# Performance work log

Measured on AMD Instinct MI355X. Metric: run time of the kernel, lower is better.

The kernel has to match this reference:

```python
import jax, jax.numpy as jnp
import numpy as np

MEM_DIM = 128  # GRU hidden / memory dim
EMB_DIM = 512  # encoder embedding dim (jk_out_channels)
N_ACTIVE = 200000
MAX_NODES = 250000
OUT_CH = 2


def setup_inputs() -> dict:
    key = jax.random.key(0)
    ks = jax.random.split(key, 8)
    s_ih = 1.0 / np.sqrt(MEM_DIM)
    return {
        "embeddings": jax.random.normal(ks[0], (N_ACTIVE, EMB_DIM), jnp.float32),
        "node_ids": jnp.arange(N_ACTIVE, dtype=jnp.int64 if jax.config.jax_enable_x64 else jnp.int32),
        "memory_bank": jax.random.normal(ks[1], (MAX_NODES, MEM_DIM), jnp.float32),
        "W_ih": jax.random.uniform(ks[2], (3 * MEM_DIM, EMB_DIM), jnp.float32, -s_ih, s_ih),
        "W_hh": jax.random.uniform(ks[3], (3 * MEM_DIM, MEM_DIM), jnp.float32, -s_ih, s_ih),
        "b_ih": jax.random.uniform(ks[4], (3 * MEM_DIM,), jnp.float32, -s_ih, s_ih),
        "b_hh": jax.random.uniform(ks[5], (3 * MEM_DIM,), jnp.float32, -s_ih, s_ih),
        "W_cls": jax.random.uniform(ks[6], (OUT_CH, EMB_DIM + MEM_DIM), jnp.float32, -1.0 / np.sqrt(EMB_DIM + MEM_DIM), 1.0 / np.sqrt(EMB_DIM + MEM_DIM)),
        "b_cls": jax.random.uniform(ks[7], (OUT_CH,), jnp.float32, -1.0 / np.sqrt(EMB_DIM + MEM_DIM), 1.0 / np.sqrt(EMB_DIM + MEM_DIM)),
    }


def gru_cell(x, h, W_ih, W_hh, b_ih, b_hh):
    # torch.nn.GRUCell math. x: [N, E], h: [N, M]
    gi = x @ W_ih.T + b_ih                 # [N, 3M]
    gh = h @ W_hh.T + b_hh                 # [N, 3M]
    i_r, i_z, i_n = jnp.split(gi, 3, axis=1)
    h_r, h_z, h_n = jnp.split(gh, 3, axis=1)
    r = jax.nn.sigmoid(i_r + h_r)
    z = jax.nn.sigmoid(i_z + h_z)
    n = jnp.tanh(i_n + r * h_n)
    return (1.0 - z) * n + z * h


def reference(embeddings, node_ids, memory_bank, W_ih, W_hh, b_ih, b_hh, W_cls, b_cls):
    # gather per-node memory
    prev_mem = memory_bank[node_ids]                       # [N, M]
    # GRUCell update
    new_mem = gru_cell(embeddings, prev_mem, W_ih, W_hh, b_ih, b_hh)
    # scatter back (detached in the original)
    updated_bank = memory_bank.at[node_ids].set(jax.lax.stop_gradient(new_mem))
    # concat + linear classify (dropout is identity at eval)
    combined = jnp.concatenate([embeddings, new_mem], axis=1)  # [N, E+M]
    logits = combined @ W_cls.T + b_cls                        # [N, out]
    return logits, updated_bank
```

## Files before the change

kernel.cpp:

```cpp
#include <hip/hip_runtime.h>
#include <hip/hip_bf16.h>

typedef short short8 __attribute__((ext_vector_type(8)));
typedef float f32x4  __attribute__((ext_vector_type(4)));

#define EMB   512
#define MEM   128
#define G3    384
#define CLS_K 640
#define KJ    640
#define BK    32
#define NKS   20
#define ROWS  64
#define NTHR  512
#define WB_CLS (G3 * KJ)

__device__ __forceinline__ short f2b(float f) {
  __hip_bfloat16 h = __float2bfloat16(f);
  return __builtin_bit_cast(short, h);
}
__device__ __forceinline__ short8 cvt8(f32x4 a, f32x4 b) {
  short8 v;
  v[0] = f2b(a[0]); v[1] = f2b(a[1]); v[2] = f2b(a[2]); v[3] = f2b(a[3]);
  v[4] = f2b(b[0]); v[5] = f2b(b[1]); v[6] = f2b(b[2]); v[7] = f2b(b[3]);
  return v;
}
__device__ __forceinline__ float sigm(float x)     { return 1.f / (1.f + __expf(-x)); }
__device__ __forceinline__ float tanhfast(float x) { return 2.f / (1.f + __expf(-2.f * x)) - 1.f; }

__device__ __forceinline__ void gll16(const void* gsrc, void* ldst) {
  __builtin_amdgcn_global_load_lds(
      (const __attribute__((address_space(1))) unsigned int*)gsrc,
      (__attribute__((address_space(3))) unsigned int*)ldst, 16, 0, 0);
}

__global__ void prep_w_kernel(const float* __restrict__ wih, const float* __restrict__ whh,
                              const float* __restrict__ wcls, short* __restrict__ outw) {
  int i = blockIdx.x * blockDim.x + threadIdx.x;
  const int nJ = G3 * KJ;
  const int nTot = nJ + 2 * EMB;
  if (i < nJ) {
    const int col = i / KJ, k = i - col * KJ;
    const float v = (k < EMB) ? wih[(size_t)col * EMB + k] : whh[(size_t)col * MEM + (k - EMB)];
    outw[i] = f2b(v);
  } else if (i < nTot) {
    const int j = i - nJ;
    const int r = j >> 9, k = j & 511;
    outw[i] = f2b(wcls[(size_t)r * CLS_K + k]);
  }
}

__global__ void bitmap_set_kernel(const int* __restrict__ ids, unsigned char* __restrict__ bm, int n) {
  int i = blockIdx.x * blockDim.x + threadIdx.x;
  if (i < n) bm[ids[i]] = 1;
}

__global__ void copy_bank_kernel(const f32x4* __restrict__ src, f32x4* __restrict__ dst,
                                 const unsigned char* __restrict__ bm, int n4) {
  int i = blockIdx.x * blockDim.x + threadIdx.x;
  int stride = gridDim.x * blockDim.x;
  for (; i < n4; i += stride) {
    if (bm && bm[i >> 5]) continue;
    dst[i] = src[i];
  }
}

template <bool BF16W>
__global__ __launch_bounds__(NTHR, 4)
void fused_gru_kernel(const float* __restrict__ emb, const int* __restrict__ ids,
                      const float* __restrict__ bank,
                      const float* __restrict__ Wihf, const float* __restrict__ Whhf,
                      const float* __restrict__ bih,  const float* __restrict__ bhh,
                      const float* __restrict__ Wcls, const float* __restrict__ bcls,
                      const short* __restrict__ Wb,
                      float* __restrict__ out_logits, float* __restrict__ out_bank, int N) {
  __shared__ __align__(16) float sA[2][ROWS * BK];
  __shared__ __align__(16) short sB[2][G3 * BK];
  __shared__ __align__(16) short sCls[2 * EMB];

  const int t    = threadIdx.x;
  const int lane = t & 63;
  const int w    = t >> 6;
  const int wr   = w & 3;
  const int wc   = w >> 2;
  const int lr   = lane & 15;
  const int lk   = lane >> 4;
  const int r0   = blockIdx.x * ROWS;

  const int rowS = w * 8 + (lane >> 3);
  const int schS = (lane & 7) ^ (rowS & 7);
  int growS = r0 + rowS; if (growS > N - 1) growS = N - 1;
  const int gidS = ids[growS];
  const char* pEmbS  = (const char*)(emb  + (size_t)growS * EMB) + schS * 16;
  const char* pBankS = (const char*)(bank + (size_t)gidS  * MEM) + schS * 16;

  int bOff[3];
#pragma unroll
  for (int s = 0; s < 3; ++s) {
    const int cB = s * 512 + w * 64 + lane;
    const int cp = cB ^ ((cB >> 3) & 7);
    bOff[s] = (cp >> 2) * KJ + (cp & 3) * 8;
  }

  if (t < 128) {
    short8 v;
    if constexpr (BF16W) v = *(const short8*)(Wb + WB_CLS + t * 8);
    else {
      const int r = t >> 6, k = (t & 63) * 8;
      const float* p = Wcls + (size_t)r * CLS_K + k;
      v = cvt8(*(const f32x4*)p, *(const f32x4*)(p + 4));
    }
    *(short8*)(sCls + t * 8) = v;
  }

  auto STAGE = [&](int kc, int buf) {
    const char* srcA = (kc < 16) ? (pEmbS + kc * 128) : (pBankS + (kc - 16) * 128);
    gll16(srcA, (char*)&sA[buf][0] + w * 1024);
    if constexpr (BF16W) {
      const short* wbk = Wb + kc * BK;
#pragma unroll
      for (int s = 0; s < 3; ++s)
        gll16((const void*)(wbk + bOff[s]), (char*)&sB[buf][0] + (s * 512 + w * 64) * 16);
    } else {
#pragma unroll
      for (int s = 0; s < 3; ++s) {
        const int g = s * 512 + w * 64 + lane;
        const int col = g >> 2, kch = g & 3;
        const int k = kc * BK + kch * 8;
        short8 v;
        if (k < EMB) { const float* p = Wihf + (size_t)col * EMB + k;         v = cvt8(*(const f32x4*)p, *(const f32x4*)(p + 4)); }
        else         { const float* p = Whhf + (size_t)col * MEM + (k - EMB); v = cvt8(*(const f32x4*)p, *(const f32x4*)(p + 4)); }
        *(short8*)((char*)&sB[buf][0] + (g ^ ((g >> 3) & 7)) * 16) = v;
      }
    }
  };

  STAGE(0, 0);
  __syncthreads();

  f32x4 accR[4], accZ[4], accIN[4], accHN[4], accL;
  const f32x4 zero = {0.f, 0.f, 0.f, 0.f};
#pragma unroll
  for (int mt = 0; mt < 4; ++mt) { accR[mt] = zero; accZ[mt] = zero; accIN[mt] = zero; accHN[mt] = zero; }
  accL = zero;

  for (int kc = 0; kc < NKS; ++kc) {
    const int buf = kc & 1;
    if (kc < NKS - 1) STAGE(kc + 1, buf ^ 1);

    const int rowA = wr * 16 + lr;
    const int ab   = rowA * 128 + lk * 32;
    const int sw   = (rowA & 7) << 4;
    const char* ap = (const char*)&sA[buf][0];
    const f32x4 av0 = *(const f32x4*)(ap + ((ab)      ^ sw));
    const f32x4 av1 = *(const f32x4*)(ap + ((ab + 16) ^ sw));
    const short8 af = cvt8(av0, av1);

    const char* bp = (const char*)&sB[buf][0];
#pragma unroll
    for (int mt = 0; mt < 4; ++mt) {
#pragma unroll
      for (int g = 0; g < 3; ++g) {
        const int col = (g * 8 + wc * 4 + mt) * 16 + lr;
        const int bb  = col * 64 + lk * 16;
        const short8 bf = *(const short8*)(bp + (bb ^ (((bb >> 7) & 7) << 4)));
        if (g == 0)      accR[mt] = __builtin_amdgcn_mfma_f32_16x16x32_bf16(af, bf, accR[mt], 0, 0, 0);
        else if (g == 1) accZ[mt] = __builtin_amdgcn_mfma_f32_16x16x32_bf16(af, bf, accZ[mt], 0, 0, 0);
        else {
          if (kc < 16) accIN[mt] = __builtin_amdgcn_mfma_f32_16x16x32_bf16(af, bf, accIN[mt], 0, 0, 0);
          else         accHN[mt] = __builtin_amdgcn_mfma_f32_16x16x32_bf16(af, bf, accHN[mt], 0, 0, 0);
        }
      }
    }
    if (wc == 0 && kc < 16) {
      short8 bqL = {0, 0, 0, 0, 0, 0, 0, 0};
      if (lr < 2) bqL = *(const short8*)(sCls + lr * 512 + kc * 32 + lk * 8);
      accL = __builtin_amdgcn_mfma_f32_16x16x32_bf16(af, bqL, accL, 0, 0, 0);
    }
    __syncthreads();
  }

  const int wrow = wr * 16;
  float* sLPp = &sA[0][0];
  float* sLEp = &sA[0][0] + 256;

  float bir[4], biz[4], bin_[4], bhn[4], wcm0[4], wcm1[4];
#pragma unroll
  for (int mt = 0; mt < 4; ++mt) {
    const int m = wc * 64 + mt * 16 + lr;
    bir[mt]  = bih[m] + bhh[m];
    biz[mt]  = bih[MEM + m] + bhh[MEM + m];
    bin_[mt] = bih[2 * MEM + m];
    bhn[mt]  = bhh[2 * MEM + m];
    wcm0[mt] = Wcls[EMB + m];
    wcm1[mt] = Wcls[CLS_K + EMB + m];
  }

  int  gidE[4]; bool valE[4];
#pragma unroll
  for (int j = 0; j < 4; ++j) {
    int gr = r0 + wrow + lk * 4 + j;
    valE[j] = gr < N; if (gr > N - 1) gr = N - 1;
    gidE[j] = ids[gr];
  }
  float hp[4][4];
#pragma unroll
  for (int j = 0; j < 4; ++j)
#pragma unroll
    for (int mt = 0; mt < 4; ++mt)
      hp[j][mt] = bank[(size_t)gidE[j] * MEM + wc * 64 + mt * 16 + lr];

#pragma unroll
  for (int j = 0; j < 4; ++j) {
    float lp0 = 0.f, lp1 = 0.f;
#pragma unroll
    for (int mt = 0; mt < 4; ++mt) {
      const int m = wc * 64 + mt * 16 + lr;
      const float rg = sigm(accR[mt][j] + bir[mt]);
      const float zg = sigm(accZ[mt][j] + biz[mt]);
      const float ng = tanhfast(accIN[mt][j] + bin_[mt] + rg * (accHN[mt][j] + bhn[mt]));
      const float nv = (1.f - zg) * ng + zg * hp[j][mt];
      if (valE[j]) out_bank[(size_t)gidE[j] * MEM + m] = nv;
      lp0 += nv * wcm0[mt];
      lp1 += nv * wcm1[mt];
    }
#pragma unroll
    for (int s = 1; s < 16; s <<= 1) {
      lp0 += __shfl_xor(lp0, s);
      lp1 += __shfl_xor(lp1, s);
    }
    const int row = wrow + lk * 4 + j;
    if (lr == 0) { sLPp[(wc * 64 + row) * 2 + 0] = lp0; sLPp[(wc * 64 + row) * 2 + 1] = lp1; }
    if (wc == 0 && lr < 2) sLEp[row * 2 + lr] = accL[j];
  }
  __syncthreads();

  if (t < 128) {
    const int row = t >> 1, c = t & 1;
    const int gr = r0 + row;
    if (gr < N)
      out_logits[(size_t)gr * 2 + c] =
          sLEp[row * 2 + c] + sLPp[row * 2 + c] + sLPp[(64 + row) * 2 + c] + bcls[c];
  }
}

extern "C" void kernel_launch(void* const* d_in, const int* in_sizes, int n_in,
                              void* d_out, int out_size, void* d_ws, size_t ws_size,
                              hipStream_t stream) {
  const float* emb  = (const float*)d_in[0];
  const int*   ids  = (const int*)d_in[1];
  const float* bank = (const float*)d_in[2];
  const float* wih  = (const float*)d_in[3];
  const float* whh  = (const float*)d_in[4];
  const float* bih  = (const float*)d_in[5];
  const float* bhh  = (const float*)d_in[6];
  const float* wcls = (const float*)d_in[7];
  const float* bcls = (const float*)d_in[8];

  const int N          = in_sizes[1];
  const int bank_elems = in_sizes[2];
  const int bank_rows  = bank_elems / MEM;
  const int n4         = bank_elems / 4;

  float* out_logits = (float*)d_out;
  float* out_bank   = (float*)d_out + (size_t)N * 2;

  const int wtot = G3 * KJ + 2 * EMB;
  const size_t wbytes  = (size_t)wtot * sizeof(short);
  const size_t bmbytes = ((size_t)bank_rows + 15) & ~15ull;

  const bool haveW  = ws_size >= wbytes;
  const bool haveBM = ws_size >= wbytes + bmbytes;

  short* wb = (short*)d_ws;
  unsigned char* bm = (unsigned char*)d_ws + wbytes;

  if (haveW)
    prep_w_kernel<<<(wtot + 255) / 256, 256, 0, stream>>>(wih, whh, wcls, wb);

  const int nb = (N + ROWS - 1) / ROWS;
  if (haveW)
    fused_gru_kernel<true><<<nb, NTHR, 0, stream>>>(emb, ids, bank, wih, whh, bih, bhh,
                                                    wcls, bcls, wb, out_logits, out_bank, N);
  else
    fused_gru_kernel<false><<<nb, NTHR, 0, stream>>>(emb, ids, bank, wih, whh, bih, bhh,
                                                     wcls, bcls, nullptr, out_logits, out_bank, N);

  if (haveBM) {
    hipMemsetAsync(bm, 0, bmbytes, stream);
    bitmap_set_kernel<<<(N + 255) / 256, 256, 0, stream>>>(ids, bm, N);
    copy_bank_kernel<<<4096, 256, 0, stream>>>((const f32x4*)bank, (f32x4*)out_bank, bm, n4);
  } else {
    copy_bank_kernel<<<4096, 256, 0, stream>>>((const f32x4*)bank, (f32x4*)out_bank, nullptr, n4);
  }
}
```

Before: 305.9 us.

## Triple-buffer GRU kernel with 32x32 MFMA tiles and coalesced LDS epilogue

Restructures the fused GRU kernel around 32x32x16 bf16 MFMA tiles with a 2x4 wave layout. Staging moves to a three-stage LDS ring, waited on with explicit vmcnt counts and a raw s_barrier instead of a per-iteration __syncthreads. The new-memory tile is staged through LDS so bank rows are written as contiguous 64-byte chunks. The classifier's memory part is computed from those rows, and its embedding part uses scalar FMAs instead of a mostly-zero MFMA. Shared memory grows to about 100 KB and launch bounds drop to 2 blocks per SM, lowering occupancy in exchange for better latency hiding and fewer LDS reads per MFMA.

Result: slower. 494.8 us (+61.8%).

```diff
diff --git a/kernel.cpp b/kernel.cpp
--- a/kernel.cpp
+++ b/kernel.cpp
@@ -3,21 +3,31 @@
 
 typedef short short8 __attribute__((ext_vector_type(8)));
 typedef float f32x4  __attribute__((ext_vector_type(4)));
+typedef float f32x16 __attribute__((ext_vector_type(16)));
 
 #define EMB   512
 #define MEM   128
 #define G3    384
 #define CLS_K 640
 #define KJ    640
-#define BK    32
 #define NKS   20
 #define ROWS  64
 #define NTHR  512
 #define WB_CLS (G3 * KJ)
 
+#define OFF_A    0
+#define OFF_B    24576
+#define OFF_CLS  98304
+#define OFF_CLSM 100352
+#define OFF_ELP  101376
+#define SMEM_SZ  101888
+
 __device__ __forceinline__ short f2b(float f) {
   __hip_bfloat16 h = __float2bfloat16(f);
   return __builtin_bit_cast(short, h);
+}
+__device__ __forceinline__ float b2f(short s) {
+  return __uint_as_float(((unsigned)(unsigned short)s) << 16);
 }
 __device__ __forceinline__ short8 cvt8(f32x4 a, f32x4 b) {
   short8 v;
@@ -65,8 +75,8 @@
   }
 }
 
-template <bool BF16W>
-__global__ __launch_bounds__(NTHR, 4)
+template <bool ASYNC>
+__global__ __launch_bounds__(NTHR, 2)
 void fused_gru_kernel(const float* __restrict__ emb, const int* __restrict__ ids,
                       const float* __restrict__ bank,
                       const float* __restrict__ Wihf, const float* __restrict__ Whhf,
@@ -74,173 +84,175 @@
                       const float* __restrict__ Wcls, const float* __restrict__ bcls,
                       const short* __restrict__ Wb,
                       float* __restrict__ out_logits, float* __restrict__ out_bank, int N) {
-  __shared__ __align__(16) float sA[2][ROWS * BK];
-  __shared__ __align__(16) short sB[2][G3 * BK];
-  __shared__ __align__(16) short sCls[2 * EMB];
-
-  const int t    = threadIdx.x;
-  const int lane = t & 63;
-  const int w    = t >> 6;
-  const int wr   = w & 3;
-  const int wc   = w >> 2;
-  const int lr   = lane & 15;
-  const int lk   = lane >> 4;
-  const int r0   = blockIdx.x * ROWS;
-
-  const int rowS = w * 8 + (lane >> 3);
-  const int schS = (lane & 7) ^ (rowS & 7);
-  int growS = r0 + rowS; if (growS > N - 1) growS = N - 1;
+  __shared__ __align__(16) char smem[SMEM_SZ];
+
+  const int t   = threadIdx.x;
+  const int l   = t & 63;
+  const int w   = t >> 6;
+  const int wr  = w >> 2;
+  const int wc  = w & 3;
+  const int lk2 = l >> 5;
+  const int l31 = l & 31;
+  const int r0  = blockIdx.x * ROWS;
+
+  int growS = r0 + l; if (growS > N - 1) growS = N - 1;
   const int gidS = ids[growS];
-  const char* pEmbS  = (const char*)(emb  + (size_t)growS * EMB) + schS * 16;
-  const char* pBankS = (const char*)(bank + (size_t)gidS  * MEM) + schS * 16;
-
-  int bOff[3];
+  const float* pEmbRow  = emb  + (size_t)growS * EMB;
+  const float* pBankRow = bank + (size_t)gidS  * MEM;
+
+  int bcol[3], bkq[3];
 #pragma unroll
   for (int s = 0; s < 3; ++s) {
-    const int cB = s * 512 + w * 64 + lane;
-    const int cp = cB ^ ((cB >> 3) & 7);
-    bOff[s] = (cp >> 2) * KJ + (cp & 3) * 8;
+    const int c = s * 512 + w * 64 + l;
+    bcol[s] = c % G3;
+    bkq[s]  = c / G3;
   }
 
   if (t < 128) {
     short8 v;
-    if constexpr (BF16W) v = *(const short8*)(Wb + WB_CLS + t * 8);
+    if constexpr (ASYNC) v = *(const short8*)(Wb + WB_CLS + t * 8);
     else {
       const int r = t >> 6, k = (t & 63) * 8;
       const float* p = Wcls + (size_t)r * CLS_K + k;
       v = cvt8(*(const f32x4*)p, *(const f32x4*)(p + 4));
     }
-    *(short8*)(sCls + t * 8) = v;
-  }
-
-  auto STAGE = [&](int kc, int buf) {
-    const char* srcA = (kc < 16) ? (pEmbS + kc * 128) : (pBankS + (kc - 16) * 128);
-    gll16(srcA, (char*)&sA[buf][0] + w * 1024);
-    if constexpr (BF16W) {
-      const short* wbk = Wb + kc * BK;
+    *(short8*)(smem + OFF_CLS + t * 16) = v;
+  } else if (t < 384) {
+    const int i = t - 128;
+    const int r = i >> 7, m = i & 127;
+    ((float*)(smem + OFF_CLSM))[r * 128 + m] = Wcls[(size_t)r * CLS_K + EMB + m];
+  }
+
+  const int mcol = wc * 32 + l31;
+  const float birv = bih[mcol] + bhh[mcol];
+  const float bizv = bih[MEM + mcol] + bhh[MEM + mcol];
+  const float binv = bih[2 * MEM + mcol];
+  const float bhnv = bhh[2 * MEM + mcol];
+
+  auto STAGE = [&](int kc) {
+    const int buf = kc % 3;
+    const float* srcA = (kc < 16) ? (pEmbRow + kc * 32 + w * 4)
+                                  : (pBankRow + (kc - 16) * 32 + w * 4);
+    gll16(srcA, smem + OFF_A + buf * 8192 + w * 1024);
+    if constexpr (ASYNC) {
 #pragma unroll
       for (int s = 0; s < 3; ++s)
-        gll16((const void*)(wbk + bOff[s]), (char*)&sB[buf][0] + (s * 512 + w * 64) * 16);
+        gll16(Wb + (size_t)bcol[s] * KJ + kc * 32 + bkq[s] * 8,
+              smem + OFF_B + buf * 24576 + (s * 512 + w * 64) * 16);
     } else {
 #pragma unroll
       for (int s = 0; s < 3; ++s) {
-        const int g = s * 512 + w * 64 + lane;
-        const int col = g >> 2, kch = g & 3;
-        const int k = kc * BK + kch * 8;
-        short8 v;
-        if (k < EMB) { const float* p = Wihf + (size_t)col * EMB + k;         v = cvt8(*(const f32x4*)p, *(const f32x4*)(p + 4)); }
-        else         { const float* p = Whhf + (size_t)col * MEM + (k - EMB); v = cvt8(*(const f32x4*)p, *(const f32x4*)(p + 4)); }
-        *(short8*)((char*)&sB[buf][0] + (g ^ ((g >> 3) & 7)) * 16) = v;
+        const int k = kc * 32 + bkq[s] * 8;
+        const float* p = (k < EMB) ? (Wihf + (size_t)bcol[s] * EMB + k)
+                                   : (Whhf + (size_t)bcol[s] * MEM + (k - EMB));
+        short8 v = cvt8(*(const f32x4*)p, *(const f32x4*)(p + 4));
+        *(short8*)(smem + OFF_B + buf * 24576 + (s * 512 + w * 64 + l) * 16) = v;
       }
     }
   };
 
-  STAGE(0, 0);
+  STAGE(0);
+  STAGE(1);
   __syncthreads();
 
-  f32x4 accR[4], accZ[4], accIN[4], accHN[4], accL;
-  const f32x4 zero = {0.f, 0.f, 0.f, 0.f};
-#pragma unroll
-  for (int mt = 0; mt < 4; ++mt) { accR[mt] = zero; accZ[mt] = zero; accIN[mt] = zero; accHN[mt] = zero; }
-  accL = zero;
+  f32x16 accR = {}, accZ = {}, accIN = {}, accHN = {};
+  float clsL0 = 0.f, clsL1 = 0.f;
+
+  const int aOff  = lk2 * 2048 + wr * 512 + l31 * 16;
+  const int bOffC = lk2 * 6144 + (wc * 32 + l31) * 16;
 
   for (int kc = 0; kc < NKS; ++kc) {
-    const int buf = kc & 1;
-    if (kc < NKS - 1) STAGE(kc + 1, buf ^ 1);
-
-    const int rowA = wr * 16 + lr;
-    const int ab   = rowA * 128 + lk * 32;
-    const int sw   = (rowA & 7) << 4;
-    const char* ap = (const char*)&sA[buf][0];
-    const f32x4 av0 = *(const f32x4*)(ap + ((ab)      ^ sw));
-    const f32x4 av1 = *(const f32x4*)(ap + ((ab + 16) ^ sw));
-    const short8 af = cvt8(av0, av1);
-
-    const char* bp = (const char*)&sB[buf][0];
-#pragma unroll
-    for (int mt = 0; mt < 4; ++mt) {
-#pragma unroll
-      for (int g = 0; g < 3; ++g) {
-        const int col = (g * 8 + wc * 4 + mt) * 16 + lr;
-        const int bb  = col * 64 + lk * 16;
-        const short8 bf = *(const short8*)(bp + (bb ^ (((bb >> 7) & 7) << 4)));
-        if (g == 0)      accR[mt] = __builtin_amdgcn_mfma_f32_16x16x32_bf16(af, bf, accR[mt], 0, 0, 0);
-        else if (g == 1) accZ[mt] = __builtin_amdgcn_mfma_f32_16x16x32_bf16(af, bf, accZ[mt], 0, 0, 0);
-        else {
-          if (kc < 16) accIN[mt] = __builtin_amdgcn_mfma_f32_16x16x32_bf16(af, bf, accIN[mt], 0, 0, 0);
-          else         accHN[mt] = __builtin_amdgcn_mfma_f32_16x16x32_bf16(af, bf, accHN[mt], 0, 0, 0);
+    const int buf = kc % 3;
+    if constexpr (ASYNC) {
+      if (kc + 1 < NKS) asm volatile("s_waitcnt vmcnt(4)" ::: "memory");
+      else              asm volatile("s_waitcnt vmcnt(0)" ::: "memory");
+      __builtin_amdgcn_s_barrier();
+      __builtin_amdgcn_sched_barrier(0);
+    } else {
+      __syncthreads();
+    }
+    if (kc + 2 < NKS) STAGE(kc + 2);
+
+    const char* ap = smem + OFF_A + buf * 8192;
+    const char* bp = smem + OFF_B + buf * 24576;
+#pragma unroll
+    for (int ks = 0; ks < 2; ++ks) {
+      const f32x4 av0 = *(const f32x4*)(ap + aOff + ks * 4096);
+      const f32x4 av1 = *(const f32x4*)(ap + aOff + ks * 4096 + 1024);
+      const short8 af = cvt8(av0, av1);
+      if (wc == 0 && kc < 16) {
+        const short8 w0 = *(const short8*)(smem + OFF_CLS + kc * 64 + ks * 32 + lk2 * 16);
+        const short8 w1 = *(const short8*)(smem + OFF_CLS + 1024 + kc * 64 + ks * 32 + lk2 * 16);
+#pragma unroll
+        for (int i = 0; i < 4; ++i) {
+          clsL0 += av0[i] * b2f(w0[i]) + av1[i] * b2f(w0[i + 4]);
+          clsL1 += av0[i] * b2f(w1[i]) + av1[i] * b2f(w1[i + 4]);
         }
       }
-    }
-    if (wc == 0 && kc < 16) {
-      short8 bqL = {0, 0, 0, 0, 0, 0, 0, 0};
-      if (lr < 2) bqL = *(const short8*)(sCls + lr * 512 + kc * 32 + lk * 8);
-      accL = __builtin_amdgcn_mfma_f32_16x16x32_bf16(af, bqL, accL, 0, 0, 0);
-    }
-    __syncthreads();
-  }
-
-  const int wrow = wr * 16;
-  float* sLPp = &sA[0][0];
-  float* sLEp = &sA[0][0] + 256;
-
-  float bir[4], biz[4], bin_[4], bhn[4], wcm0[4], wcm1[4];
-#pragma unroll
-  for (int mt = 0; mt < 4; ++mt) {
-    const int m = wc * 64 + mt * 16 + lr;
-    bir[mt]  = bih[m] + bhh[m];
-    biz[mt]  = bih[MEM + m] + bhh[MEM + m];
-    bin_[mt] = bih[2 * MEM + m];
-    bhn[mt]  = bhh[2 * MEM + m];
-    wcm0[mt] = Wcls[EMB + m];
-    wcm1[mt] = Wcls[CLS_K + EMB + m];
-  }
-
-  int  gidE[4]; bool valE[4];
-#pragma unroll
-  for (int j = 0; j < 4; ++j) {
-    int gr = r0 + wrow + lk * 4 + j;
-    valE[j] = gr < N; if (gr > N - 1) gr = N - 1;
-    gidE[j] = ids[gr];
-  }
-  float hp[4][4];
-#pragma unroll
-  for (int j = 0; j < 4; ++j)
-#pragma unroll
-    for (int mt = 0; mt < 4; ++mt)
-      hp[j][mt] = bank[(size_t)gidE[j] * MEM + wc * 64 + mt * 16 + lr];
-
-#pragma unroll
-  for (int j = 0; j < 4; ++j) {
+      const short8 b0 = *(const short8*)(bp + bOffC + ks * 12288);
+      const short8 b1 = *(const short8*)(bp + bOffC + ks * 12288 + 2048);
+      const short8 b2 = *(const short8*)(bp + bOffC + ks * 12288 + 4096);
+      accR = __builtin_amdgcn_mfma_f32_32x32x16_bf16(af, b0, accR, 0, 0, 0);
+      accZ = __builtin_amdgcn_mfma_f32_32x32x16_bf16(af, b1, accZ, 0, 0, 0);
+      if (kc < 16) accIN = __builtin_amdgcn_mfma_f32_32x32x16_bf16(af, b2, accIN, 0, 0, 0);
+      else         accHN = __builtin_amdgcn_mfma_f32_32x32x16_bf16(af, b2, accHN, 0, 0, 0);
+    }
+  }
+  __syncthreads();
+
+  float* nvT = (float*)smem;
+  float hp[16];
+#pragma unroll
+  for (int j = 0; j < 16; ++j) {
+    const int row32 = (j & 3) + 8 * (j >> 2) + 4 * lk2;
+    const int gid = __shfl(gidS, wr * 32 + row32);
+    hp[j] = bank[(size_t)gid * MEM + mcol];
+  }
+#pragma unroll
+  for (int j = 0; j < 16; ++j) {
+    const int row32 = (j & 3) + 8 * (j >> 2) + 4 * lk2;
+    const int row = wr * 32 + row32;
+    const float rg = sigm(accR[j] + birv);
+    const float zg = sigm(accZ[j] + bizv);
+    const float ng = tanhfast(accIN[j] + binv + rg * (accHN[j] + bhnv));
+    nvT[row * 132 + mcol] = (1.f - zg) * ng + zg * hp[j];
+  }
+  if (wc == 0) {
+    const float e0 = clsL0 + __shfl_xor(clsL0, 32);
+    const float e1 = clsL1 + __shfl_xor(clsL1, 32);
+    if (l < 32) {
+      float* elp = (float*)(smem + OFF_ELP);
+      elp[(wr * 32 + l) * 2 + 0] = e0;
+      elp[(wr * 32 + l) * 2 + 1] = e1;
+    }
+  }
+  __syncthreads();
+
+  {
+    const int row = t >> 3, q = t & 7;
+    const int gid = __shfl(gidS, row);
+    const f32x4 v0 = *(const f32x4*)(nvT + row * 132 + q * 16);
+    const f32x4 v1 = *(const f32x4*)(nvT + row * 132 + q * 16 + 4);
+    const f32x4 v2 = *(const f32x4*)(nvT + row * 132 + q * 16 + 8);
+    const f32x4 v3 = *(const f32x4*)(nvT + row * 132 + q * 16 + 12);
+    float* dst = out_bank + (size_t)gid * MEM + q * 16;
+    *(f32x4*)dst = v0; *(f32x4*)(dst + 4) = v1; *(f32x4*)(dst + 8) = v2; *(f32x4*)(dst + 12) = v3;
+
+    const float* cm0 = (const float*)(smem + OFF_CLSM) + q * 16;
+    const float* cm1 = (const float*)(smem + OFF_CLSM) + 128 + q * 16;
     float lp0 = 0.f, lp1 = 0.f;
 #pragma unroll
-    for (int mt = 0; mt < 4; ++mt) {
-      const int m = wc * 64 + mt * 16 + lr;
-      const float rg = sigm(accR[mt][j] + bir[mt]);
-      const float zg = sigm(accZ[mt][j] + biz[mt]);
-      const float ng = tanhfast(accIN[mt][j] + bin_[mt] + rg * (accHN[mt][j] + bhn[mt]));
-      const float nv = (1.f - zg) * ng + zg * hp[j][mt];
-      if (valE[j]) out_bank[(size_t)gidE[j] * MEM + m] = nv;
-      lp0 += nv * wcm0[mt];
-      lp1 += nv * wcm1[mt];
-    }
-#pragma unroll
-    for (int s = 1; s < 16; s <<= 1) {
-      lp0 += __shfl_xor(lp0, s);
-      lp1 += __shfl_xor(lp1, s);
-    }
-    const int row = wrow + lk * 4 + j;
-    if (lr == 0) { sLPp[(wc * 64 + row) * 2 + 0] = lp0; sLPp[(wc * 64 + row) * 2 + 1] = lp1; }
-    if (wc == 0 && lr < 2) sLEp[row * 2 + lr] = accL[j];
-  }
-  __syncthreads();
-
-  if (t < 128) {
-    const int row = t >> 1, c = t & 1;
-    const int gr = r0 + row;
-    if (gr < N)
-      out_logits[(size_t)gr * 2 + c] =
-          sLEp[row * 2 + c] + sLPp[row * 2 + c] + sLPp[(64 + row) * 2 + c] + bcls[c];
+    for (int i = 0; i < 4; ++i) {
+      lp0 += v0[i] * cm0[i] + v1[i] * cm0[4 + i] + v2[i] * cm0[8 + i] + v3[i] * cm0[12 + i];
+      lp1 += v0[i] * cm1[i] + v1[i] * cm1[4 + i] + v2[i] * cm1[8 + i] + v3[i] * cm1[12 + i];
+    }
+#pragma unroll
+    for (int s = 1; s < 8; s <<= 1) { lp0 += __shfl_xor(lp0, s); lp1 += __shfl_xor(lp1, s); }
+    if (q == 0 && r0 + row < N) {
+      const float* elp = (const float*)(smem + OFF_ELP);
+      out_logits[(size_t)(r0 + row) * 2 + 0] = lp0 + elp[row * 2 + 0] + bcls[0];
+      out_logits[(size_t)(r0 + row) * 2 + 1] = lp1 + elp[row * 2 + 1] + bcls[1];
+    }
   }
 }
 
```
